# Performance work log

Hardware: AMD Instinct MI355X
Metric: run time of the kernel (lower is better)

Reference implementation:

```python
import jax, jax.numpy as jnp
import numpy as np

D_MODEL = 1024
NUM_HEADS = 16
D_K = D_MODEL // NUM_HEADS
FFN_SIZE = 4096
EPS = 1e-6


def _layer_norm(x, gamma, beta):
    mu = jnp.mean(x, axis=-1, keepdims=True)
    var = jnp.var(x, axis=-1, keepdims=True)
    return (x - mu) / jnp.sqrt(var + EPS) * gamma + beta


def setup_inputs() -> dict:
    key = jax.random.key(0)
    ks = jax.random.split(key, 12)
    B, S = 2, 2048
    s_attn = 1.0 / np.sqrt(D_MODEL)
    s_ffn1 = 1.0 / np.sqrt(D_MODEL)
    s_ffn2 = 1.0 / np.sqrt(FFN_SIZE)
    return {
        "x": jax.random.normal(ks[0], (B, S, D_MODEL), dtype=jnp.float32),
        "W_q": jax.random.normal(ks[1], (D_MODEL, D_MODEL), dtype=jnp.float32) * s_attn,
        "W_k": jax.random.normal(ks[2], (D_MODEL, D_MODEL), dtype=jnp.float32) * s_attn,
        "W_v": jax.random.normal(ks[3], (D_MODEL, D_MODEL), dtype=jnp.float32) * s_attn,
        "W_o": jax.random.normal(ks[4], (D_MODEL, D_MODEL), dtype=jnp.float32) * s_attn,
        "b_o": jnp.zeros((D_MODEL,), dtype=jnp.float32),
        "W1": jax.random.normal(ks[5], (D_MODEL, FFN_SIZE), dtype=jnp.float32) * s_ffn1,
        "b1": jnp.zeros((FFN_SIZE,), dtype=jnp.float32),
        "W2": jax.random.normal(ks[6], (FFN_SIZE, D_MODEL), dtype=jnp.float32) * s_ffn2,
        "b2": jnp.zeros((D_MODEL,), dtype=jnp.float32),
        "ln1_g": jnp.ones((D_MODEL,), dtype=jnp.float32),
        "ln1_b": jnp.zeros((D_MODEL,), dtype=jnp.float32),
        "ln2_g": jnp.ones((D_MODEL,), dtype=jnp.float32),
        "ln2_b": jnp.zeros((D_MODEL,), dtype=jnp.float32),
    }


def reference(x, W_q, W_k, W_v, W_o, b_o, W1, b1, W2, b2,
              ln1_g, ln1_b, ln2_g, ln2_b):
    B, S, _ = x.shape

    # --- self-attention sublayer (pre-norm residual) ---
    h = _layer_norm(x, ln1_g, ln1_b)
    q = (h @ W_q).reshape(B, S, NUM_HEADS, D_K).transpose(0, 2, 1, 3)  # [B,H,S,Dk]
    k = (h @ W_k).reshape(B, S, NUM_HEADS, D_K).transpose(0, 2, 1, 3)
    v = (h @ W_v).reshape(B, S, NUM_HEADS, D_K).transpose(0, 2, 1, 3)
    scores = jnp.einsum("bhqd,bhkd->bhqk", q, k) / jnp.sqrt(jnp.float32(D_K))
    attn = jax.nn.softmax(scores, axis=-1)
    ctx = jnp.einsum("bhqk,bhkd->bhqd", attn, v)
    ctx = ctx.transpose(0, 2, 1, 3).reshape(B, S, D_MODEL)
    x = x + (ctx @ W_o + b_o)

    # --- FFN sublayer (pre-norm residual) ---
    h2 = _layer_norm(x, ln2_g, ln2_b)
    f = jax.nn.relu(h2 @ W1 + b1) @ W2 + b2
    return x + f
```

## Files before the change

### kernel.cpp

```cpp
#include <hip/hip_runtime.h>
#include <cstdint>
#include <cstddef>


typedef __attribute__((ext_vector_type(8))) __bf16 bf16x8;
typedef __attribute__((ext_vector_type(4))) __bf16 bf16x4;
typedef __attribute__((ext_vector_type(4))) float f32x4;

__device__ __forceinline__ void async16(const void* g, void* l) {
  __builtin_amdgcn_global_load_lds(
      (__attribute__((address_space(1))) void*)g,
      (__attribute__((address_space(3))) void*)l, 16, 0, 0);
}

__device__ __forceinline__ f32x4 mfma16(bf16x8 a, bf16x8 b, f32x4 c) {
  return __builtin_amdgcn_mfma_f32_16x16x32_bf16(a, b, c, 0, 0, 0);
}

template <int N>
__device__ __forceinline__ void wait_vmcnt() {
  if constexpr (N == 0) {
    asm volatile("s_waitcnt vmcnt(0)" ::: "memory");
  } else if constexpr (N == 3) {
    asm volatile("s_waitcnt vmcnt(3)" ::: "memory");
  } else {
    asm volatile("s_waitcnt vmcnt(4)" ::: "memory");
  }
}
__device__ __forceinline__ void barrier_raw() {
  asm volatile("s_barrier" ::: "memory");
}

__device__ __forceinline__ void ln_body(const float* __restrict__ xin,
                                        const float* __restrict__ g,
                                        const float* __restrict__ bt,
                                        __bf16* __restrict__ out, int tok,
                                        int lane) {
  const int base0 = lane * 8, base1 = 512 + lane * 8;
  const float* xr = xin + (size_t)tok * 1024;
  float v[16];
  float4 a0 = *(const float4*)(xr + base0);
  float4 a1 = *(const float4*)(xr + base0 + 4);
  float4 a2 = *(const float4*)(xr + base1);
  float4 a3 = *(const float4*)(xr + base1 + 4);
  v[0] = a0.x; v[1] = a0.y; v[2] = a0.z; v[3] = a0.w;
  v[4] = a1.x; v[5] = a1.y; v[6] = a1.z; v[7] = a1.w;
  v[8] = a2.x; v[9] = a2.y; v[10] = a2.z; v[11] = a2.w;
  v[12] = a3.x; v[13] = a3.y; v[14] = a3.z; v[15] = a3.w;
  float s = 0.f, s2 = 0.f;
#pragma unroll
  for (int i = 0; i < 16; i++) { s += v[i]; s2 += v[i] * v[i]; }
#pragma unroll
  for (int m = 1; m < 64; m <<= 1) {
    s += __shfl_xor(s, m);
    s2 += __shfl_xor(s2, m);
  }
  const float mean = s * (1.f / 1024.f);
  const float var = s2 * (1.f / 1024.f) - mean * mean;
  const float rstd = rsqrtf(var + 1e-6f);
  float4 g0 = *(const float4*)(g + base0), g1 = *(const float4*)(g + base0 + 4);
  float4 g2 = *(const float4*)(g + base1), g3 = *(const float4*)(g + base1 + 4);
  float4 b0 = *(const float4*)(bt + base0), b1v = *(const float4*)(bt + base0 + 4);
  float4 b2v = *(const float4*)(bt + base1), b3 = *(const float4*)(bt + base1 + 4);
  float gg[16] = {g0.x, g0.y, g0.z, g0.w, g1.x, g1.y, g1.z, g1.w,
                  g2.x, g2.y, g2.z, g2.w, g3.x, g3.y, g3.z, g3.w};
  float bb[16] = {b0.x, b0.y, b0.z, b0.w, b1v.x, b1v.y, b1v.z, b1v.w,
                  b2v.x, b2v.y, b2v.z, b2v.w, b3.x, b3.y, b3.z, b3.w};
  bf16x8 o0, o1;
#pragma unroll
  for (int j = 0; j < 8; j++) {
    o0[j] = (__bf16)((v[j] - mean) * rstd * gg[j] + bb[j]);
    o1[j] = (__bf16)((v[8 + j] - mean) * rstd * gg[8 + j] + bb[8 + j]);
  }
  __bf16* op = out + (size_t)tok * 1024;
  *(bf16x8*)(op + base0) = o0;
  *(bf16x8*)(op + base1) = o1;
}

__global__ __launch_bounds__(256) void prep_kernel(
    const float* __restrict__ Wq, const float* __restrict__ Wk,
    const float* __restrict__ Wv, const float* __restrict__ Wo,
    const float* __restrict__ W1, const float* __restrict__ W2,
    const float* __restrict__ x, const float* __restrict__ ln1g,
    const float* __restrict__ ln1b, __bf16* __restrict__ WqkvT,
    __bf16* __restrict__ WoT, __bf16* __restrict__ W1T,
    __bf16* __restrict__ W2T, __bf16* __restrict__ h) {
  const int id = blockIdx.x;
  if (id >= 3072) {
    const int tok = (id - 3072) * 4 + (threadIdx.x >> 6);
    ln_body(x, ln1g, ln1b, h, tok, threadIdx.x & 63);
    return;
  }
  const float* in;
  __bf16* out;
  int ld_in, ld_out, c0, r0;
  if (id < 1024) {
    const int which = id >> 8, tl = id & 255;
    c0 = (tl & 15) * 64;
    r0 = (tl >> 4) * 64;
    ld_in = 1024;
    ld_out = 1024;
    if (which == 0) { in = Wq; out = WqkvT; }
    else if (which == 1) { in = Wk; out = WqkvT + 1048576; }
    else if (which == 2) { in = Wv; out = WqkvT + 2097152; }
    else { in = Wo; out = WoT; }
  } else if (id < 2048) {
    const int tl = id - 1024;
    c0 = (tl & 63) * 64;
    r0 = (tl >> 6) * 64;
    in = W1; out = W1T; ld_in = 4096; ld_out = 1024;
  } else {
    const int tl = id - 2048;
    c0 = (tl & 15) * 64;
    r0 = (tl >> 4) * 64;
    in = W2; out = W2T; ld_in = 1024; ld_out = 4096;
  }
  __shared__ __bf16 tile[64][65];
  const int tx = threadIdx.x & 63, ty = threadIdx.x >> 6;
#pragma unroll
  for (int i = 0; i < 16; i++) {
    int r = ty + i * 4;
    tile[r][tx] = (__bf16)in[(size_t)(r0 + r) * ld_in + c0 + tx];
  }
  __syncthreads();
#pragma unroll
  for (int i = 0; i < 16; i++) {
    int r = ty + i * 4;
    out[(size_t)(c0 + r) * ld_out + r0 + tx] = tile[tx][r];
  }
}

__global__ __launch_bounds__(256) void ln_kernel(
    const float* __restrict__ xin, const float* __restrict__ g,
    const float* __restrict__ bt, __bf16* __restrict__ out) {
  const int tok = blockIdx.x * 4 + (threadIdx.x >> 6);
  ln_body(xin, g, bt, out, tok, threadIdx.x & 63);
}

template <int EPI, int SPLITS = 1>
__global__ __launch_bounds__(512, 2) void gemm256(
    const __bf16* __restrict__ A, int lda, const __bf16* __restrict__ BT,
    int ldb, void* __restrict__ C, int ldc, int Kb,
    const float* __restrict__ bias, __bf16* __restrict__ VTout) {
  const int t = threadIdx.x;
  const int m0 = blockIdx.x * 256, n0 = blockIdx.y * 256;
  const int kz = (SPLITS > 1) ? blockIdx.z : 0;
  __shared__ __align__(16) __bf16 As[2][2][8192];
  __shared__ __align__(16) __bf16 Bs[2][2][8192];
  const int lane = t & 63;
  const int quad = lane >> 4, l15 = lane & 15;
  const int w = t >> 6, wm = w >> 2, wn = w & 3;

  f32x4 acc[8][4] = {};

  const int rr = t >> 3;
  const int ca = (t & 7) ^ (rr & 7);
  const int cc = rr & 31;
  const int wnb = t >> 8;
  const int cb = (t & 7) ^ (cc & 7);
  const __bf16* gA = A + (size_t)kz * Kb + (size_t)(m0 + rr) * lda + ca * 8;
  const __bf16* gB = BT + (size_t)kz * Kb +
                     (size_t)(n0 + wnb * 64 + cc) * ldb + cb * 8;
  const size_t a64 = (size_t)64 * lda, a128 = (size_t)128 * lda;
  const size_t b32 = (size_t)32 * ldb, b128 = (size_t)128 * ldb;

  auto stageA = [&](int buf, int mq, int ko) {
    const __bf16* g = gA + (mq ? a64 : 0) + ko;
    __bf16* l = &As[buf][mq][t * 8];
    async16(g, l);
    async16(g + a128, l + 4096);
  };
  auto stageB = [&](int buf, int nq, int ko) {
    const __bf16* g = gB + (nq ? b32 : 0) + ko;
    __bf16* l = &Bs[buf][nq][t * 8];
    async16(g, l);
    async16(g + b128, l + 4096);
  };

  const int arow = wm * 4096 + l15 * 64;
  const int brow = wn * 2048 + l15 * 64;
  const int x7 = l15 & 7;

  auto loadA = [&](int buf, int mq, bf16x8 (&af)[4][2]) {
#pragma unroll
    for (int mi = 0; mi < 4; mi++)
#pragma unroll
      for (int kk = 0; kk < 2; kk++)
        af[mi][kk] = *(const bf16x8*)&As[buf][mq]
            [arow + mi * 1024 + (((kk * 4 + quad) ^ x7) * 8)];
  };
  auto loadB = [&](int buf, int nq, bf16x8 (&bv)[2][2]) {
#pragma unroll
    for (int ni = 0; ni < 2; ni++)
#pragma unroll
      for (int kk = 0; kk < 2; kk++)
        bv[ni][kk] = *(const bf16x8*)&Bs[buf][nq]
            [brow + ni * 1024 + (((kk * 4 + quad) ^ x7) * 8)];
  };
  auto mm = [&](int mq, int nq, const bf16x8 (&af)[4][2],
                const bf16x8 (&bv)[2][2]) {
    __builtin_amdgcn_s_setprio(1);
#pragma unroll
    for (int mi = 0; mi < 4; mi++)
#pragma unroll
      for (int ni = 0; ni < 2; ni++)
#pragma unroll
        for (int kk = 0; kk < 2; kk++)
          acc[mq * 4 + mi][nq * 2 + ni] =
              mfma16(af[mi][kk], bv[ni][kk], acc[mq * 4 + mi][nq * 2 + ni]);
    __builtin_amdgcn_s_setprio(0);
  };

  const int NT = Kb / 64;
  stageA(0, 0, 0); stageB(0, 0, 0); stageA(0, 1, 0); stageB(0, 1, 0);
  stageA(1, 0, 64); stageB(1, 0, 64);
  wait_vmcnt<4>();
  barrier_raw();

  bf16x8 af[4][2], b0[2][2], b1[2][2];
  for (int s = 0; s < NT; ++s) {
    const int buf = s & 1;
    const int ko1 = (s + 1) * 64, ko2 = (s + 2) * 64;
    loadA(buf, 0, af);
    loadB(buf, 0, b0);
    loadB(buf, 1, b1);
    if (s + 1 < NT) {
      stageA(buf ^ 1, 1, ko1);
      stageB(buf ^ 1, 1, ko1);
    }
    mm(0, 0, af, b0);
    mm(0, 1, af, b1);
    barrier_raw();
    loadA(buf, 1, af);
    if (s + 2 < NT) {
      stageA(buf, 0, ko2);
      stageB(buf, 0, ko2);
      wait_vmcnt<4>();
    } else {
      wait_vmcnt<0>();
    }
    mm(1, 0, af, b0);
    mm(1, 1, af, b1);
    barrier_raw();
  }

  if constexpr (EPI == 3) {
    if (n0 >= 2048) {
      const int colb = m0 + wm * 128;
#pragma unroll
      for (int mi = 0; mi < 8; mi++) {
        const int tcol = colb + (mi >> 1) * 32 + quad * 8 + (mi & 1) * 4;
#pragma unroll
        for (int ni = 0; ni < 4; ni++) {
          const int vrow = n0 - 2048 + wn * 64 + ni * 16 + l15;
          bf16x4 o;
#pragma unroll
          for (int r = 0; r < 4; r++) o[r] = (__bf16)acc[mi][ni][r];
          *(bf16x4*)&VTout[(size_t)vrow * 4096 + tcol] = o;
        }
      }
      return;
    }
  }

  float biasv[4];
  if constexpr (EPI == 2) {
#pragma unroll
    for (int ni = 0; ni < 4; ni++)
      biasv[ni] = bias[n0 + wn * 64 + ni * 16 + l15];
  }
  __bf16* Cb = (__bf16*)C;
  if constexpr (SPLITS > 1)
    Cb += (size_t)kz * (size_t)gridDim.x * 256 * ldc;
#pragma unroll
  for (int mi = 0; mi < 8; mi++)
#pragma unroll
    for (int ni = 0; ni < 4; ni++)
#pragma unroll
      for (int r = 0; r < 4; r++) {
        const int row = m0 + wm * 128 + mi * 16 + quad * 4 + r;
        const int col = n0 + wn * 64 + ni * 16 + l15;
        float v = acc[mi][ni][r];
        if constexpr (EPI == 0 || EPI == 3) {
          Cb[(size_t)row * ldc + col] = (__bf16)v;
        } else {
          v += biasv[ni];
          Cb[(size_t)row * ldc + col] = (__bf16)fmaxf(v, 0.f);
        }
      }
}

template <int EPI, int TM, int SPLITS = 1>
__global__ __launch_bounds__(256) void gemm_bt(
    const __bf16* __restrict__ A, int lda, const __bf16* __restrict__ BT,
    int ldb, void* __restrict__ C, int ldc, int Kb,
    const float* __restrict__ bias, const float* __restrict__ res, int ldres) {
  const int t = threadIdx.x;
  const int m0 = blockIdx.x * TM, n0 = blockIdx.y * 128;
  const int kz = (SPLITS > 1) ? blockIdx.z : 0;
  __shared__ __align__(16) __bf16 As[3][TM * 32];
  __shared__ __align__(16) __bf16 Bs[3][128 * 32];
  const int lane = t & 63, w = t >> 6;
  const int quad = lane >> 4, l15 = lane & 15;
  const int wm = w >> 1, wn = w & 1;
  constexpr int MF = TM / 32;
  constexpr int LOADS = TM / 64 + 2;

  f32x4 acc[MF][4] = {};

  const int swc = ((t & 3) ^ ((t >> 3) & 3)) * 8;
  const __bf16* ga = A + (size_t)(m0 + (t >> 2)) * lda + swc + (size_t)kz * Kb;
  const __bf16* gb = BT + (size_t)(n0 + (t >> 2)) * ldb + swc + (size_t)kz * Kb;
  const size_t a64 = (size_t)64 * lda, b64 = (size_t)64 * ldb;

  auto stage = [&](int buf) {
#pragma unroll
    for (int i = 0; i < TM / 64; i++)
      async16(ga + i * a64, As[buf] + t * 8 + i * 2048);
    async16(gb, Bs[buf] + t * 8);
    async16(gb + b64, Bs[buf] + t * 8 + 2048);
    ga += 32;
    gb += 32;
  };
  const int ce = (quad ^ ((l15 >> 1) & 3)) * 8;
  auto compute = [&](int buf) {
    bf16x8 af[MF], bfr[4];
#pragma unroll
    for (int i = 0; i < MF; i++)
      af[i] = *(const bf16x8*)&As[buf][(wm * (TM / 2) + i * 16 + l15) * 32 + ce];
#pragma unroll
    for (int i = 0; i < 4; i++)
      bfr[i] = *(const bf16x8*)&Bs[buf][(wn * 64 + i * 16 + l15) * 32 + ce];
#pragma unroll
    for (int mi = 0; mi < MF; mi++)
#pragma unroll
      for (int ni = 0; ni < 4; ni++)
        acc[mi][ni] = mfma16(af[mi], bfr[ni], acc[mi][ni]);
  };

  const int iters = Kb / 32;
  stage(0);
  stage(1);
  int cur = 0, stg = 2;
  for (int it = 0; it < iters - 1; ++it) {
    wait_vmcnt<LOADS>();
    barrier_raw();
    if (it + 2 < iters) stage(stg);
    compute(cur);
    cur = (cur == 2) ? 0 : cur + 1;
    stg = (stg == 2) ? 0 : stg + 1;
  }
  wait_vmcnt<0>();
  barrier_raw();
  compute(cur);

  float biasv[4];
  if constexpr (EPI != 0) {
#pragma unroll
    for (int ni = 0; ni < 4; ni++)
      biasv[ni] = bias[n0 + wn * 64 + ni * 16 + l15];
  }
  __bf16* Cb = (__bf16*)C;
  if constexpr (SPLITS > 1)
    Cb += (size_t)kz * gridDim.x * TM * ldc;
#pragma unroll
  for (int mi = 0; mi < MF; mi++)
#pragma unroll
    for (int ni = 0; ni < 4; ni++)
#pragma unroll
      for (int r = 0; r < 4; r++) {
        const int row = m0 + wm * (TM / 2) + mi * 16 + quad * 4 + r;
        const int col = n0 + wn * 64 + ni * 16 + l15;
        float v = acc[mi][ni][r];
        if constexpr (EPI == 0) {
          Cb[(size_t)row * ldc + col] = (__bf16)v;
        } else if constexpr (EPI == 1) {
          v += biasv[ni] + res[(size_t)row * ldres + col];
          ((float*)C)[(size_t)row * ldc + col] = v;
        } else {
          v += biasv[ni];
          ((__bf16*)C)[(size_t)row * ldc + col] = (__bf16)fmaxf(v, 0.f);
        }
      }
}

__global__ __launch_bounds__(256) void reduce_split4(
    const __bf16* __restrict__ P, const float* __restrict__ bias,
    const float* __restrict__ res, float* __restrict__ out) {
  const int row = blockIdx.x, c = threadIdx.x * 4;
  const size_t i = (size_t)row * 1024 + c;
  float4 r = *(const float4*)(res + i);
  float4 bv = *(const float4*)(bias + c);
  float s0 = r.x + bv.x, s1 = r.y + bv.y, s2 = r.z + bv.z, s3 = r.w + bv.w;
#pragma unroll
  for (int j = 0; j < 4; j++) {
    bf16x4 p = *(const bf16x4*)(P + (size_t)j * 4194304 + i);
    s0 += (float)p[0];
    s1 += (float)p[1];
    s2 += (float)p[2];
    s3 += (float)p[3];
  }
  float4 o = {s0, s1, s2, s3};
  *(float4*)(out + i) = o;
}

__global__ __launch_bounds__(256, 2) void attn_kernel(
    const __bf16* __restrict__ QKV, const __bf16* __restrict__ VT,
    __bf16* __restrict__ ctx) {
  const int id = blockIdx.x;
  const int xg = id & 7, idx = id >> 3;
  const int bh = xg * 4 + (idx & 3);
  const int qt = idx >> 2;
  const int b = bh >> 4, h = bh & 15;
  const int t = threadIdx.x, w = t >> 6, lane = t & 63;
  const int quad = lane >> 4, l15 = lane & 15;
  const int tok0 = b * 2048;
  const int q0w = tok0 + qt * 128 + w * 32;

  __shared__ __align__(16) __bf16 Ks[2][128 * 64];
  __shared__ __align__(16) __bf16 VTs[2][64 * 128];

  const float qs = 0.18033688011112042f;
  bf16x8 qf[2][2];
#pragma unroll
  for (int mi = 0; mi < 2; mi++)
#pragma unroll
    for (int kb = 0; kb < 2; kb++) {
      const __bf16* src = QKV + (size_t)(q0w + mi * 16 + l15) * 3072 + h * 64 +
                          kb * 32 + quad * 8;
      bf16x8 r = *(const bf16x8*)src;
#pragma unroll
      for (int j = 0; j < 8; j++) r[j] = (__bf16)((float)r[j] * qs);
      qf[mi][kb] = r;
    }

  bf16x8 onesv;
#pragma unroll
  for (int j = 0; j < 8; j++) onesv[j] = (__bf16)1.0f;

  f32x4 O[2][4] = {};
  f32x4 Ol[2] = {};

  const int krow = t >> 3;
  const int kcg = (((t & 7) ^ (krow & 7)) * 8);
  const int vrow = t >> 4;
  const int vcg = (((t & 15) ^ (vrow & 7)) * 8);
  const int x7 = l15 & 7;

  auto stage = [&](int buf, int kt) {
    const int ktok = tok0 + kt * 128;
#pragma unroll
    for (int j = 0; j < 4; j++) {
      const __bf16* gp =
          QKV + (size_t)(ktok + krow + j * 32) * 3072 + 1024 + h * 64 + kcg;
      async16(gp, Ks[buf] + t * 8 + j * 2048);
    }
#pragma unroll
    for (int j = 0; j < 4; j++) {
      const __bf16* gp =
          VT + (size_t)(h * 64 + vrow + j * 16) * 4096 + ktok + vcg;
      async16(gp, VTs[buf] + t * 8 + j * 2048);
    }
  };

  stage(0, 0);
  wait_vmcnt<0>();
  barrier_raw();

  int buf = 0;
  for (int kt = 0; kt < 16; ++kt) {
    if (kt + 1 < 16) stage(buf ^ 1, kt + 1);

    f32x4 sT[2][8];
    auto qkblk = [&](int kb) {
      __builtin_amdgcn_s_setprio(1);
#pragma unroll
      for (int kt8 = 2 * kb; kt8 < 2 * kb + 2; kt8++) {
        f32x4 a0 = {}, a1 = {};
#pragma unroll
        for (int kq = 0; kq < 2; kq++) {
          bf16x8 kf = *(const bf16x8*)&Ks[buf][(kt8 * 16 + l15) * 64 +
                                              (((kq * 4 + quad) ^ x7) * 8)];
          a0 = mfma16(kf, qf[0][kq], a0);
          a1 = mfma16(kf, qf[1][kq], a1);
        }
        sT[0][kt8] = a0;
        sT[1][kt8] = a1;
      }
      __builtin_amdgcn_s_setprio(0);
    };

    qkblk(0);
#pragma unroll
    for (int kb = 0; kb < 4; kb++) {
      if (kb < 3) qkblk(kb + 1);
      bf16x8 pf0, pf1;
#pragma unroll
      for (int hf = 0; hf < 2; hf++)
#pragma unroll
        for (int r = 0; r < 4; r++) {
          const float p0 = __builtin_amdgcn_exp2f(sT[0][2 * kb + hf][r]);
          const float p1 = __builtin_amdgcn_exp2f(sT[1][2 * kb + hf][r]);
          pf0[hf * 4 + r] = (__bf16)p0;
          pf1[hf * 4 + r] = (__bf16)p1;
        }
      __builtin_amdgcn_s_setprio(1);
#pragma unroll
      for (int nd = 0; nd < 4; nd++) {
        bf16x8 vf = *(const bf16x8*)&VTs[buf][(nd * 16 + l15) * 128 +
                                             (((4 * kb + quad) ^ x7) * 8)];
        O[0][nd] = mfma16(pf0, vf, O[0][nd]);
        O[1][nd] = mfma16(pf1, vf, O[1][nd]);
      }
      Ol[0] = mfma16(pf0, onesv, Ol[0]);
      Ol[1] = mfma16(pf1, onesv, Ol[1]);
      __builtin_amdgcn_s_setprio(0);
    }

    wait_vmcnt<0>();
    barrier_raw();
    buf ^= 1;
  }

#pragma unroll
  for (int mi = 0; mi < 2; mi++) {
    float rl[4];
#pragma unroll
    for (int r = 0; r < 4; r++) rl[r] = 1.0f / Ol[mi][r];
#pragma unroll
    for (int nd = 0; nd < 4; nd++)
#pragma unroll
      for (int r = 0; r < 4; r++) {
        const int tokq = q0w + mi * 16 + quad * 4 + r;
        const int col = h * 64 + nd * 16 + l15;
        ctx[(size_t)tokq * 1024 + col] = (__bf16)(O[mi][nd][r] * rl[r]);
      }
  }
}

extern "C" void kernel_launch(void* const* d_in, const int* in_sizes, int n_in,
                              void* d_out, int out_size, void* d_ws,
                              size_t ws_size, hipStream_t stream) {
  (void)in_sizes; (void)n_in; (void)out_size; (void)ws_size;

  const float* x = (const float*)d_in[0];
  const float* Wq = (const float*)d_in[1];
  const float* Wk = (const float*)d_in[2];
  const float* Wv = (const float*)d_in[3];
  const float* Wo = (const float*)d_in[4];
  const float* b_o = (const float*)d_in[5];
  const float* W1 = (const float*)d_in[6];
  const float* b1 = (const float*)d_in[7];
  const float* W2 = (const float*)d_in[8];
  const float* b2 = (const float*)d_in[9];
  const float* ln1g = (const float*)d_in[10];
  const float* ln1b = (const float*)d_in[11];
  const float* ln2g = (const float*)d_in[12];
  const float* ln2b = (const float*)d_in[13];

  char* ws = (char*)d_ws;
  __bf16* h = (__bf16*)(ws + 0);
  __bf16* W1T = (__bf16*)(ws + 8388608);
  __bf16* WqkvT = (__bf16*)(ws + 16777216);
  __bf16* WoT = (__bf16*)(ws + 23068672);
  __bf16* QKV = (__bf16*)(ws + 25165824);
  __bf16* VT = (__bf16*)(ws + 50331648);
  __bf16* ctx = (__bf16*)(ws + 58720256);
  __bf16* f1 = (__bf16*)(ws + 33554432);
  __bf16* Pw2 = (__bf16*)(ws + 0);
  float* x1 = (float*)(ws + 67108864);
  __bf16* W2T = (__bf16*)(ws + 83886080);

  const dim3 blk(256);
  const dim3 blk512(512);

  prep_kernel<<<dim3(4096), blk, 0, stream>>>(Wq, Wk, Wv, Wo, W1, W2, x, ln1g,
                                              ln1b, WqkvT, WoT, W1T, W2T, h);

  gemm256<3><<<dim3(16, 12), blk512, 0, stream>>>(
      h, 1024, WqkvT, 1024, (void*)QKV, 3072, 1024, nullptr, VT);

  attn_kernel<<<dim3(512), blk, 0, stream>>>(QKV, VT, ctx);

  gemm_bt<1, 64><<<dim3(64, 8), blk, 0, stream>>>(
      ctx, 1024, WoT, 1024, (void*)x1, 1024, 1024, b_o, x, 1024);

  ln_kernel<<<dim3(1024), blk, 0, stream>>>(x1, ln2g, ln2b, h);

  gemm256<2><<<dim3(16, 16), blk512, 0, stream>>>(
      h, 1024, W1T, 1024, (void*)f1, 4096, 1024, b1, nullptr);

  gemm256<0, 4><<<dim3(16, 4, 4), blk512, 0, stream>>>(
      f1, 4096, W2T, 4096, (void*)Pw2, 1024, 1024, nullptr, nullptr);
  reduce_split4<<<dim3(4096), blk, 0, stream>>>(Pw2, b2, x1, (float*)d_out);
}
```

Measured before the change: 297.8 us.

## Replace split-K partial buffers and reduce kernel with atomic accumulation into output

The second layer-norm kernel now also initializes the output with residual plus b2. The split-K W2 GEMM then atomically adds its fp32 partial sums straight into the output, so the bf16 partial buffer and the separate reduce kernel are gone. This saves one launch and the partial write and read traffic. In exchange it issues many scalar fp32 atomics, 4 per element, which may contend, and the summation order becomes nondeterministic.

```diff
diff --git a/kernel.cpp b/kernel.cpp
--- a/kernel.cpp
+++ b/kernel.cpp
@@ -130,11 +130,62 @@
   }
 }
 
-__global__ __launch_bounds__(256) void ln_kernel(
+__global__ __launch_bounds__(256) void ln2init_kernel(
     const float* __restrict__ xin, const float* __restrict__ g,
-    const float* __restrict__ bt, __bf16* __restrict__ out) {
+    const float* __restrict__ bt, const float* __restrict__ b2,
+    __bf16* __restrict__ out, float* __restrict__ dout) {
   const int tok = blockIdx.x * 4 + (threadIdx.x >> 6);
-  ln_body(xin, g, bt, out, tok, threadIdx.x & 63);
+  const int lane = threadIdx.x & 63;
+  const int base0 = lane * 8, base1 = 512 + lane * 8;
+  const float* xr = xin + (size_t)tok * 1024;
+  float v[16];
+  float4 a0 = *(const float4*)(xr + base0);
+  float4 a1 = *(const float4*)(xr + base0 + 4);
+  float4 a2 = *(const float4*)(xr + base1);
+  float4 a3 = *(const float4*)(xr + base1 + 4);
+  v[0] = a0.x; v[1] = a0.y; v[2] = a0.z; v[3] = a0.w;
+  v[4] = a1.x; v[5] = a1.y; v[6] = a1.z; v[7] = a1.w;
+  v[8] = a2.x; v[9] = a2.y; v[10] = a2.z; v[11] = a2.w;
+  v[12] = a3.x; v[13] = a3.y; v[14] = a3.z; v[15] = a3.w;
+  float s = 0.f, s2 = 0.f;
+#pragma unroll
+  for (int i = 0; i < 16; i++) { s += v[i]; s2 += v[i] * v[i]; }
+#pragma unroll
+  for (int m = 1; m < 64; m <<= 1) {
+    s += __shfl_xor(s, m);
+    s2 += __shfl_xor(s2, m);
+  }
+  const float mean = s * (1.f / 1024.f);
+  const float var = s2 * (1.f / 1024.f) - mean * mean;
+  const float rstd = rsqrtf(var + 1e-6f);
+  float4 g0 = *(const float4*)(g + base0), g1 = *(const float4*)(g + base0 + 4);
+  float4 g2 = *(const float4*)(g + base1), g3 = *(const float4*)(g + base1 + 4);
+  float4 b0 = *(const float4*)(bt + base0), b1v = *(const float4*)(bt + base0 + 4);
+  float4 b2v = *(const float4*)(bt + base1), b3 = *(const float4*)(bt + base1 + 4);
+  float gg[16] = {g0.x, g0.y, g0.z, g0.w, g1.x, g1.y, g1.z, g1.w,
+                  g2.x, g2.y, g2.z, g2.w, g3.x, g3.y, g3.z, g3.w};
+  float bb[16] = {b0.x, b0.y, b0.z, b0.w, b1v.x, b1v.y, b1v.z, b1v.w,
+                  b2v.x, b2v.y, b2v.z, b2v.w, b3.x, b3.y, b3.z, b3.w};
+  bf16x8 o0, o1;
+#pragma unroll
+  for (int j = 0; j < 8; j++) {
+    o0[j] = (__bf16)((v[j] - mean) * rstd * gg[j] + bb[j]);
+    o1[j] = (__bf16)((v[8 + j] - mean) * rstd * gg[8 + j] + bb[8 + j]);
+  }
+  __bf16* op = out + (size_t)tok * 1024;
+  *(bf16x8*)(op + base0) = o0;
+  *(bf16x8*)(op + base1) = o1;
+  float4 c0v = *(const float4*)(b2 + base0), c1 = *(const float4*)(b2 + base0 + 4);
+  float4 c2 = *(const float4*)(b2 + base1), c3 = *(const float4*)(b2 + base1 + 4);
+  float* dp = dout + (size_t)tok * 1024;
+  float4 d0 = {v[0] + c0v.x, v[1] + c0v.y, v[2] + c0v.z, v[3] + c0v.w};
+  float4 d1 = {v[4] + c1.x, v[5] + c1.y, v[6] + c1.z, v[7] + c1.w};
+  float4 d2 = {v[8] + c2.x, v[9] + c2.y, v[10] + c2.z, v[11] + c2.w};
+  float4 d3 = {v[12] + c3.x, v[13] + c3.y, v[14] + c3.z, v[15] + c3.w};
+  *(float4*)(dp + base0) = d0;
+  *(float4*)(dp + base0 + 4) = d1;
+  *(float4*)(dp + base1) = d2;
+  *(float4*)(dp + base1 + 4) = d3;
 }
 
 template <int EPI, int SPLITS = 1>
@@ -263,6 +314,21 @@
     }
   }
 
+  if constexpr (EPI == 4) {
+    float* Cf = (float*)C;
+#pragma unroll
+    for (int mi = 0; mi < 8; mi++)
+#pragma unroll
+      for (int ni = 0; ni < 4; ni++)
+#pragma unroll
+        for (int r = 0; r < 4; r++) {
+          const int row = m0 + wm * 128 + mi * 16 + quad * 4 + r;
+          const int col = n0 + wn * 64 + ni * 16 + l15;
+          unsafeAtomicAdd(&Cf[(size_t)row * ldc + col], acc[mi][ni][r]);
+        }
+    return;
+  }
+
   float biasv[4];
   if constexpr (EPI == 2) {
 #pragma unroll
@@ -270,8 +336,6 @@
       biasv[ni] = bias[n0 + wn * 64 + ni * 16 + l15];
   }
   __bf16* Cb = (__bf16*)C;
-  if constexpr (SPLITS > 1)
-    Cb += (size_t)kz * (size_t)gridDim.x * 256 * ldc;
 #pragma unroll
   for (int mi = 0; mi < 8; mi++)
 #pragma unroll
@@ -384,26 +448,6 @@
       }
 }
 
-__global__ __launch_bounds__(256) void reduce_split4(
-    const __bf16* __restrict__ P, const float* __restrict__ bias,
-    const float* __restrict__ res, float* __restrict__ out) {
-  const int row = blockIdx.x, c = threadIdx.x * 4;
-  const size_t i = (size_t)row * 1024 + c;
-  float4 r = *(const float4*)(res + i);
-  float4 bv = *(const float4*)(bias + c);
-  float s0 = r.x + bv.x, s1 = r.y + bv.y, s2 = r.z + bv.z, s3 = r.w + bv.w;
-#pragma unroll
-  for (int j = 0; j < 4; j++) {
-    bf16x4 p = *(const bf16x4*)(P + (size_t)j * 4194304 + i);
-    s0 += (float)p[0];
-    s1 += (float)p[1];
-    s2 += (float)p[2];
-    s3 += (float)p[3];
-  }
-  float4 o = {s0, s1, s2, s3};
-  *(float4*)(out + i) = o;
-}
-
 __global__ __launch_bounds__(256, 2) void attn_kernel(
     const __bf16* __restrict__ QKV, const __bf16* __restrict__ VT,
     __bf16* __restrict__ ctx) {
@@ -567,7 +611,6 @@
   __bf16* VT = (__bf16*)(ws + 50331648);
   __bf16* ctx = (__bf16*)(ws + 58720256);
   __bf16* f1 = (__bf16*)(ws + 33554432);
-  __bf16* Pw2 = (__bf16*)(ws + 0);
   float* x1 = (float*)(ws + 67108864);
   __bf16* W2T = (__bf16*)(ws + 83886080);
 
@@ -585,12 +628,12 @@
   gemm_bt<1, 64><<<dim3(64, 8), blk, 0, stream>>>(
       ctx, 1024, WoT, 1024, (void*)x1, 1024, 1024, b_o, x, 1024);
 
-  ln_kernel<<<dim3(1024), blk, 0, stream>>>(x1, ln2g, ln2b, h);
+  ln2init_kernel<<<dim3(1024), blk, 0, stream>>>(x1, ln2g, ln2b, b2, h,
+                                                 (float*)d_out);
 
   gemm256<2><<<dim3(16, 16), blk512, 0, stream>>>(
       h, 1024, W1T, 1024, (void*)f1, 4096, 1024, b1, nullptr);
 
-  gemm256<0, 4><<<dim3(16, 4, 4), blk512, 0, stream>>>(
-      f1, 4096, W2T, 4096, (void*)Pw2, 1024, 1024, nullptr, nullptr);
-  reduce_split4<<<dim3(4096), blk, 0, stream>>>(Pw2, b2, x1, (float*)d_out);
-}
+  gemm256<4, 4><<<dim3(16, 4, 4), blk512, 0, stream>>>(
+      f1, 4096, W2T, 4096, (void*)d_out, 1024, 1024, nullptr, nullptr);
+}
```

Result: slower. 324.4 us (+8.9%).
